# Kernel tuning notes

Measured on AMD Instinct MI355X. Metric: run time of the kernel, lower is better.

## Reference

```python
import jax, jax.numpy as jnp
import numpy as np

NUM_NODES = 94
SEQ_LEN = 784
OUT_CLASSES = 10
ALPHA = 0.5
GAMMA = 0.1
OMEGA = 2.0 * np.pi / 28.0
H = 1.0
INV_SQRT_N = 1.0 / np.sqrt(NUM_NODES)


def _xavier(key, shape):
    fan_in, fan_out = shape[1], shape[0]
    limit = np.sqrt(6.0 / (fan_in + fan_out))
    return jax.random.uniform(key, shape, jnp.float32, -limit, limit)


def setup_inputs() -> dict:
    key = jax.random.key(0)
    k_in, k_ih, k_hh, k_ro = jax.random.split(key, 4)
    batch = 1024
    return {
        "input_sequence": jax.random.normal(k_in, (batch, SEQ_LEN), jnp.float32),
        "w_ih": _xavier(k_ih, (NUM_NODES, 1)),   # Linear(1 -> N) weight
        "b_ih": jnp.zeros((NUM_NODES,), jnp.float32),
        "w_hh": _xavier(k_hh, (NUM_NODES, NUM_NODES)),  # Linear(N -> N) weight
        "b_hh": jnp.zeros((NUM_NODES,), jnp.float32),
        "w_ro": _xavier(k_ro, (OUT_CLASSES, NUM_NODES)),  # readout weight
        "b_ro": jnp.zeros((OUT_CLASSES,), jnp.float32),
    }


def reference(input_sequence, w_ih, b_ih, w_hh, b_hh, w_ro, b_ro):
    batch = input_sequence.shape[0]
    # precompute external drive for all steps: [T, B, N]
    # W_ih(s_t) with input_dim=1 is an outer product: s_t * w_ih[:,0] + b_ih
    s = input_sequence.T  # [T, B]
    w_ih_vec = w_ih[:, 0]  # [N]

    def step(carry, s_t):
        x, y = carry
        I_ext = s_t[:, None] * w_ih_vec[None, :] + b_ih  # [B, N]
        I_rec = y @ w_hh.T + b_hh                        # [B, N]
        A = (I_ext + I_rec) * INV_SQRT_N
        accel = ALPHA * jnp.tanh(A) - 2.0 * GAMMA * y - (OMEGA ** 2) * x
        x_new = x + H * y
        y_new = y + H * accel
        return (x_new, y_new), None

    x0 = jnp.zeros((batch, NUM_NODES), jnp.float32)
    y0 = jnp.zeros((batch, NUM_NODES), jnp.float32)
    (x_final, _), _ = jax.lax.scan(step, (x0, y0), s)
    return x_final @ w_ro.T + b_ro  # [B, 10]
```

## Files before the change

kernel.cpp:

```cpp
#include <hip/hip_runtime.h>
#include <math.h>

#define NUM_NODES 94
#define SEQ_LEN 784
#define OUT_CLASSES 10

#define TWO_GAMMA 0.2f
#define OM2 0.0503551324598949f
#define INV_SQRT_N 0.103142124625879
#define LOG2E 1.4426950408889634
#define WSCALE ((float)(2.0 * INV_SQRT_N * LOG2E))

typedef float f2 __attribute__((ext_vector_type(2)));
typedef float f4 __attribute__((ext_vector_type(4)));

__device__ __forceinline__ float dpp_xor1(float x) {
    return __int_as_float(__builtin_amdgcn_mov_dpp(__float_as_int(x), 0xB1, 0xF, 0xF, true));
}
__device__ __forceinline__ float dpp_xor2(float x) {
    return __int_as_float(__builtin_amdgcn_mov_dpp(__float_as_int(x), 0x4E, 0xF, 0xF, true));
}
__device__ __forceinline__ float dpp_mir8(float x) {
    return __int_as_float(__builtin_amdgcn_mov_dpp(__float_as_int(x), 0x141, 0xF, 0xF, true));
}

__global__
__attribute__((amdgpu_flat_work_group_size(64, 64), amdgpu_waves_per_eu(1, 1)))
void horn_kernel(
    const float* __restrict__ input,
    const float* __restrict__ w_ih,
    const float* __restrict__ b_ih,
    const float* __restrict__ w_hh,
    const float* __restrict__ b_hh,
    const float* __restrict__ w_ro,
    const float* __restrict__ b_ro,
    float* __restrict__ out)
{
    __shared__ __align__(16) float ysh[96];

    const int lane = threadIdx.x;
    const int g    = lane >> 3;
    const int lw   = lane & 7;
    const int bb   = blockIdx.x;

    const int b0  = lane & 1, b1 = (lane >> 1) & 1, b2v = (lane >> 2) & 1;
    const bool c0 = ((b0 ^ b2v) != 0);
    const bool c1 = ((b1 ^ b2v) != 0);
    const bool c2 = (b2v != 0);

    const int row0 = 12 * g, col0 = 12 * lw;
    f2 w2[12][6];
    #pragma unroll
    for (int i = 0; i < 12; i++) {
        const int rr = row0 + i;
        #pragma unroll
        for (int c = 0; c < 12; c++) {
            const int cc = col0 + c;
            float v = (rr < NUM_NODES && cc < NUM_NODES)
                        ? w_hh[rr * NUM_NODES + cc] * WSCALE : 0.0f;
            w2[i][c >> 1][c & 1] = v;
        }
    }

    const int nA = row0 + 4 * b2v + 2 * (b1 ^ b2v) + (b0 ^ b2v);
    const int nB = row0 + 8 + 2 * (b1 ^ b2v) + (b0 ^ b2v);
    const float wihA  = (nA < NUM_NODES) ? w_ih[nA] * WSCALE : 0.0f;
    const float biasA = (nA < NUM_NODES) ? (b_ih[nA] + b_hh[nA]) * WSCALE : 0.0f;
    const float wihB  = (nB < NUM_NODES) ? w_ih[nB] * WSCALE : 0.0f;
    const float biasB = (nB < NUM_NODES) ? (b_ih[nB] + b_hh[nB]) * WSCALE : 0.0f;

    float xA = 0.0f, yA = 0.0f, xB = 0.0f, yB = 0.0f;

    const float* srow = input + (size_t)bb * SEQ_LEN;
    float sc = srow[0];

    const f4* yv = (const f4*)&ysh[col0];

    for (int t = 0; t < SEQ_LEN; t++) {
        const int tn = (t + 1 < SEQ_LEN) ? t + 1 : (SEQ_LEN - 1);
        float sn = srow[tn];

        ysh[nA] = yA;
        ysh[nB] = yB;
        asm volatile("s_waitcnt lgkmcnt(0)" ::: "memory");
        f4 Y0 = yv[0], Y1 = yv[1], Y2 = yv[2];
        f2 yy0 = __builtin_shufflevector(Y0, Y0, 0, 1);
        f2 yy1 = __builtin_shufflevector(Y0, Y0, 2, 3);
        f2 yy2 = __builtin_shufflevector(Y1, Y1, 0, 1);
        f2 yy3 = __builtin_shufflevector(Y1, Y1, 2, 3);
        f2 yy4 = __builtin_shufflevector(Y2, Y2, 0, 1);
        f2 yy5 = __builtin_shufflevector(Y2, Y2, 2, 3);

        f2 P[12];
        #pragma unroll
        for (int i = 0; i < 12; i++) {
            f2 p = w2[i][0] * yy0;
            p += w2[i][1] * yy1;  p += w2[i][2] * yy2;
            p += w2[i][3] * yy3;  p += w2[i][4] * yy4;
            p += w2[i][5] * yy5;
            P[i] = p;
        }
        float P0 = P[0][0] + P[0][1],   P1 = P[1][0] + P[1][1];
        float P2 = P[2][0] + P[2][1],   P3 = P[3][0] + P[3][1];
        float P4 = P[4][0] + P[4][1],   P5 = P[5][0] + P[5][1];
        float P6 = P[6][0] + P[6][1],   P7 = P[7][0] + P[7][1];
        float P8 = P[8][0] + P[8][1],   P9 = P[9][0] + P[9][1];
        float P10 = P[10][0] + P[10][1], P11 = P[11][0] + P[11][1];

        float Q0 = (c0 ? P1 : P0) + dpp_xor1(c0 ? P0 : P1);
        float Q1 = (c0 ? P3 : P2) + dpp_xor1(c0 ? P2 : P3);
        float Q2 = (c0 ? P5 : P4) + dpp_xor1(c0 ? P4 : P5);
        float Q3 = (c0 ? P7 : P6) + dpp_xor1(c0 ? P6 : P7);
        float Q4 = (c0 ? P9 : P8) + dpp_xor1(c0 ? P8 : P9);
        float Q5 = (c0 ? P11 : P10) + dpp_xor1(c0 ? P10 : P11);
        float R0 = (c1 ? Q1 : Q0) + dpp_xor2(c1 ? Q0 : Q1);
        float R1 = (c1 ? Q3 : Q2) + dpp_xor2(c1 ? Q2 : Q3);
        float R2 = (c1 ? Q5 : Q4) + dpp_xor2(c1 ? Q4 : Q5);
        float SA = (c2 ? R1 : R0) + dpp_mir8(c2 ? R0 : R1);
        float SB = R2 + dpp_mir8(R2);

        float eA = __builtin_amdgcn_exp2f(fmaf(sc, wihA, biasA) + SA);
        float aA = 0.5f - __builtin_amdgcn_rcpf(eA + 1.0f);
        aA = fmaf(-TWO_GAMMA, yA, aA);
        aA = fmaf(-OM2, xA, aA);
        xA += yA;  yA += aA;

        float eB = __builtin_amdgcn_exp2f(fmaf(sc, wihB, biasB) + SB);
        float aB = 0.5f - __builtin_amdgcn_rcpf(eB + 1.0f);
        aB = fmaf(-TWO_GAMMA, yB, aB);
        aB = fmaf(-OM2, xB, aB);
        xB += yB;  yB += aB;

        sc = sn;
    }

    ysh[nA] = xA;
    ysh[nB] = xB;
    asm volatile("s_waitcnt lgkmcnt(0)" ::: "memory");

    if (lane < OUT_CLASSES) {
        float acc = b_ro[lane];
        #pragma unroll 2
        for (int j = 0; j < NUM_NODES; j++) {
            acc += ysh[j] * w_ro[lane * NUM_NODES + j];
        }
        out[(size_t)bb * OUT_CLASSES + lane] = acc;
    }
}

extern "C" void kernel_launch(void* const* d_in, const int* in_sizes, int n_in,
                              void* d_out, int out_size, void* d_ws, size_t ws_size,
                              hipStream_t stream) {
    const float* input = (const float*)d_in[0];
    const float* w_ih  = (const float*)d_in[1];
    const float* b_ih  = (const float*)d_in[2];
    const float* w_hh  = (const float*)d_in[3];
    const float* b_hh  = (const float*)d_in[4];
    const float* w_ro  = (const float*)d_in[5];
    const float* b_ro  = (const float*)d_in[6];
    float* out = (float*)d_out;

    const int batch = in_sizes[0] / SEQ_LEN;
    dim3 grid(batch);
    dim3 block(64);

    hipLaunchKernelGGL(horn_kernel, grid, block, 0, stream,
                       input, w_ih, b_ih, w_hh, b_hh, w_ro, b_ro, out);
}
```

Measured before the change: 358.0 us.

## Split recurrent matvec columns across two waves with LDS partial-sum exchange

Each batch element now gets a 128-thread block. Each of the two waves holds half of the recurrent weight columns and computes partial row sums. The partials are swapped through double-buffered shared memory with a block barrier every timestep, and both waves then update the full oscillator state redundantly. The aim is to shorten the per-step dependency chain by halving each wave's FMA work. The cost is a __syncthreads per step and twice as many waves competing for the same SIMDs.

Measured after the change: 504.1 us. 1.41x slower.

```diff
diff --git a/kernel.cpp b/kernel.cpp
--- a/kernel.cpp
+++ b/kernel.cpp
@@ -4,6 +4,7 @@
 #define NUM_NODES 94
 #define SEQ_LEN 784
 #define OUT_CLASSES 10
+#define THREADS 128
 
 #define TWO_GAMMA 0.2f
 #define OM2 0.0503551324598949f
@@ -12,7 +13,6 @@
 #define WSCALE ((float)(2.0 * INV_SQRT_N * LOG2E))
 
 typedef float f2 __attribute__((ext_vector_type(2)));
-typedef float f4 __attribute__((ext_vector_type(4)));
 
 __device__ __forceinline__ float dpp_xor1(float x) {
     return __int_as_float(__builtin_amdgcn_mov_dpp(__float_as_int(x), 0xB1, 0xF, 0xF, true));
@@ -25,7 +25,7 @@
 }
 
 __global__
-__attribute__((amdgpu_flat_work_group_size(64, 64), amdgpu_waves_per_eu(1, 1)))
+__attribute__((amdgpu_flat_work_group_size(THREADS, THREADS), amdgpu_waves_per_eu(2, 2)))
 void horn_kernel(
     const float* __restrict__ input,
     const float* __restrict__ w_ih,
@@ -36,9 +36,12 @@
     const float* __restrict__ b_ro,
     float* __restrict__ out)
 {
-    __shared__ __align__(16) float ysh[96];
+    __shared__ __align__(16) float ysh[2][96];
+    __shared__ __align__(16) float psh[2][2][96];
 
-    const int lane = threadIdx.x;
+    const int tid  = threadIdx.x;
+    const int wv   = tid >> 6;
+    const int lane = tid & 63;
     const int g    = lane >> 3;
     const int lw   = lane & 7;
     const int bb   = blockIdx.x;
@@ -48,13 +51,14 @@
     const bool c1 = ((b1 ^ b2v) != 0);
     const bool c2 = (b2v != 0);
 
-    const int row0 = 12 * g, col0 = 12 * lw;
-    f2 w2[12][6];
+    const int row0 = 12 * g;
+    const int col0 = 48 * wv + 6 * lw;
+    f2 w2[12][3];
     #pragma unroll
     for (int i = 0; i < 12; i++) {
         const int rr = row0 + i;
         #pragma unroll
-        for (int c = 0; c < 12; c++) {
+        for (int c = 0; c < 6; c++) {
             const int cc = col0 + c;
             float v = (rr < NUM_NODES && cc < NUM_NODES)
                         ? w_hh[rr * NUM_NODES + cc] * WSCALE : 0.0f;
@@ -71,33 +75,27 @@
 
     float xA = 0.0f, yA = 0.0f, xB = 0.0f, yB = 0.0f;
 
+    ysh[wv][nA] = 0.0f;
+    ysh[wv][nB] = 0.0f;
+    __syncthreads();
+
     const float* srow = input + (size_t)bb * SEQ_LEN;
     float sc = srow[0];
 
-    const f4* yv = (const f4*)&ysh[col0];
+    const f2* yv = (const f2*)&ysh[wv][col0];
 
     for (int t = 0; t < SEQ_LEN; t++) {
         const int tn = (t + 1 < SEQ_LEN) ? t + 1 : (SEQ_LEN - 1);
         float sn = srow[tn];
 
-        ysh[nA] = yA;
-        ysh[nB] = yB;
-        asm volatile("s_waitcnt lgkmcnt(0)" ::: "memory");
-        f4 Y0 = yv[0], Y1 = yv[1], Y2 = yv[2];
-        f2 yy0 = __builtin_shufflevector(Y0, Y0, 0, 1);
-        f2 yy1 = __builtin_shufflevector(Y0, Y0, 2, 3);
-        f2 yy2 = __builtin_shufflevector(Y1, Y1, 0, 1);
-        f2 yy3 = __builtin_shufflevector(Y1, Y1, 2, 3);
-        f2 yy4 = __builtin_shufflevector(Y2, Y2, 0, 1);
-        f2 yy5 = __builtin_shufflevector(Y2, Y2, 2, 3);
+        f2 yy0 = yv[0], yy1 = yv[1], yy2 = yv[2];
 
         f2 P[12];
         #pragma unroll
         for (int i = 0; i < 12; i++) {
             f2 p = w2[i][0] * yy0;
-            p += w2[i][1] * yy1;  p += w2[i][2] * yy2;
-            p += w2[i][3] * yy3;  p += w2[i][4] * yy4;
-            p += w2[i][5] * yy5;
+            p += w2[i][1] * yy1;
+            p += w2[i][2] * yy2;
             P[i] = p;
         }
         float P0 = P[0][0] + P[0][1],   P1 = P[1][0] + P[1][1];
@@ -119,6 +117,13 @@
         float SA = (c2 ? R1 : R0) + dpp_mir8(c2 ? R0 : R1);
         float SB = R2 + dpp_mir8(R2);
 
+        const int pp = t & 1;
+        psh[pp][wv][nA] = SA;
+        psh[pp][wv][nB] = SB;
+        __syncthreads();
+        SA += psh[pp][wv ^ 1][nA];
+        SB += psh[pp][wv ^ 1][nB];
+
         float eA = __builtin_amdgcn_exp2f(fmaf(sc, wihA, biasA) + SA);
         float aA = 0.5f - __builtin_amdgcn_rcpf(eA + 1.0f);
         aA = fmaf(-TWO_GAMMA, yA, aA);
@@ -131,20 +136,26 @@
         aB = fmaf(-OM2, xB, aB);
         xB += yB;  yB += aB;
 
+        ysh[wv][nA] = yA;
+        ysh[wv][nB] = yB;
+        asm volatile("s_waitcnt lgkmcnt(0)" ::: "memory");
+
         sc = sn;
     }
 
-    ysh[nA] = xA;
-    ysh[nB] = xB;
+    if (wv == 0) {
+        psh[0][0][nA] = xA;
+        psh[0][0][nB] = xB;
+    }
     asm volatile("s_waitcnt lgkmcnt(0)" ::: "memory");
 
-    if (lane < OUT_CLASSES) {
-        float acc = b_ro[lane];
+    if (tid < OUT_CLASSES) {
+        float acc = b_ro[tid];
         #pragma unroll 2
         for (int j = 0; j < NUM_NODES; j++) {
-            acc += ysh[j] * w_ro[lane * NUM_NODES + j];
+            acc += psh[0][0][j] * w_ro[tid * NUM_NODES + j];
         }
-        out[(size_t)bb * OUT_CLASSES + lane] = acc;
+        out[(size_t)bb * OUT_CLASSES + tid] = acc;
     }
 }
 
@@ -162,7 +173,7 @@
 
     const int batch = in_sizes[0] / SEQ_LEN;
     dim3 grid(batch);
-    dim3 block(64);
+    dim3 block(THREADS);
 
     hipLaunchKernelGGL(horn_kernel, grid, block, 0, stream,
                        input, w_ih, b_ih, w_hh, b_hh, w_ro, b_ro, out);
```
